# Performance work log

Measured on AMD Instinct MI355X. Metric: run time of the kernel, lower is better.

## Reference

```python
import jax, jax.numpy as jnp
import numpy as np

THETA_BASE = 10000.0

def rope(x, pos_offset=0):
    # x: (B, S, D), D even. Rotates interleaved (even, odd) dim pairs.
    B, S, D = x.shape
    pos = jnp.arange(pos_offset, pos_offset + S, dtype=jnp.float32)[:, None]  # (S,1)
    p = jnp.arange(D // 2, dtype=jnp.float32)  # p-1 in source, 0-indexed here
    theta = pos * (THETA_BASE ** (-2.0 * p / D))  # (S, D//2)
    sin_t, cos_t = jnp.sin(theta), jnp.cos(theta)
    x1, x2 = x[..., 0::2], x[..., 1::2]
    r1 = x1 * cos_t - x2 * sin_t
    r2 = x1 * sin_t + x2 * cos_t
    return jnp.stack((r1, r2), axis=-1).reshape(B, S, D)

def setup_inputs() -> dict:
    key = jax.random.key(0)
    k1, k2, k3, k4 = jax.random.split(key, 4)
    B, S, E, Dh = 4, 4096, 2048, 128
    return {
        "x": jax.random.normal(k1, (B, S, E), dtype=jnp.float32),
        "W_Q": jax.random.normal(k2, (E, Dh), dtype=jnp.float32) / np.sqrt(E),
        "W_K": jax.random.normal(k3, (E, Dh), dtype=jnp.float32) / np.sqrt(E),
        "W_V": jax.random.normal(k4, (E, Dh), dtype=jnp.float32) / np.sqrt(E),
    }

def reference(x, W_Q, W_K, W_V):
    d_h = W_Q.shape[1]
    past_len = 0  # kv_cache is None (prefill)
    Q = rope(x @ W_Q, pos_offset=past_len)  # NOTE: source ropes Q and V, not K
    K = x @ W_K
    V = rope(x @ W_V, pos_offset=past_len)
    scores = jnp.einsum('bqd,bkd->bqk', Q, K) / jnp.sqrt(jnp.float32(d_h))
    S_q, S_total = scores.shape[-2], scores.shape[-1]
    i = jnp.arange(S_q)[:, None] + past_len
    j = jnp.arange(S_total)[None, :]
    causal = j <= i  # (S_q, S_total) bool
    masked = jnp.where(causal[None, :, :], scores, jnp.float32(-jnp.inf))
    attn = jax.nn.softmax(masked, axis=-1)
    return jnp.einsum('bqk,bkd->bqd', attn, V)
```

## Files before the change

kernel.cpp:

```cpp
#include <hip/hip_runtime.h>
#include <hip/hip_bf16.h>
#include <stdint.h>

#define S_LEN 4096
#define E_DIM 2048
#define DH    128

typedef __bf16 bf16_t;
typedef bf16_t bf16x8 __attribute__((ext_vector_type(8)));
typedef float  f32x4  __attribute__((ext_vector_type(4)));

__device__ __forceinline__ unsigned short f2bf(float f) {
  union { float f; uint32_t u; } v; v.f = f;
  uint32_t u = v.u;
  uint32_t r = (u + 0x7fffu + ((u >> 16) & 1u)) >> 16;
  return (unsigned short)r;
}

__device__ __forceinline__ bf16x8 ld_bf16x8(const unsigned short* p) {
  return *(const bf16x8*)p;
}

__device__ __forceinline__ f32x4 mfma16(bf16x8 a, bf16x8 b, f32x4 c) {
  return __builtin_amdgcn_mfma_f32_16x16x32_bf16(a, b, c, 0, 0, 0);
}

__device__ __forceinline__ void gload16(const void* gsrc, void* ldst) {
  __builtin_amdgcn_global_load_lds(
      (const __attribute__((address_space(1))) uint32_t*)gsrc,
      (__attribute__((address_space(3))) uint32_t*)ldst, 16, 0, 0);
}

__global__ __launch_bounds__(256) void prep_kernel(
    const float* __restrict__ WQ, const float* __restrict__ WK,
    const float* __restrict__ WV,
    float2* __restrict__ trig, unsigned short* __restrict__ Wt)
{
  const int bx  = blockIdx.x;
  const int tid = threadIdx.x;
  if (bx < 1024) {
    const int idx = bx * 256 + tid;
    const int pos = idx >> 6, p = idx & 63;
    const float freq = powf(10000.0f, -(float)p / 64.0f);
    float sv, cv;
    sincosf((float)pos * freq, &sv, &cv);
    trig[idx] = make_float2(cv, sv);
    return;
  }
  __shared__ float lds[64][65];
  const int t   = bx - 1024;
  const int z   = t >> 6;
  const int rem = t & 63;
  const int k0  = (rem >> 1) * 64;
  const int n0  = (rem & 1) * 64;
  const float* W = (z == 0) ? WQ : ((z == 1) ? WK : WV);
  #pragma unroll
  for (int pass = 0; pass < 4; pass++) {
    const int r  = pass * 16 + (tid >> 4);
    const int c4 = (tid & 15) * 4;
    float4 v = *(const float4*)(W + (size_t)(k0 + r) * 128 + n0 + c4);
    lds[c4 + 0][r] = v.x; lds[c4 + 1][r] = v.y;
    lds[c4 + 2][r] = v.z; lds[c4 + 3][r] = v.w;
  }
  __syncthreads();
  #pragma unroll
  for (int pass = 0; pass < 4; pass++) {
    const int n  = pass * 16 + (tid >> 4);
    const int k4 = (tid & 15) * 4;
    ushort4 pk;
    pk.x = f2bf(lds[n][k4 + 0]); pk.y = f2bf(lds[n][k4 + 1]);
    pk.z = f2bf(lds[n][k4 + 2]); pk.w = f2bf(lds[n][k4 + 3]);
    *(ushort4*)(Wt + (size_t)(z * 128 + n0 + n) * E_DIM + k0 + k4) = pk;
  }
}

__global__ __launch_bounds__(256, 3) void proj_kernel(
    const float* __restrict__ x, const unsigned short* __restrict__ Wt,
    const float2* __restrict__ trig,
    unsigned short* __restrict__ Qb, unsigned short* __restrict__ Kb,
    unsigned short* __restrict__ Vt)
{
  __shared__ __align__(16) uint8_t Abuf[2 * 128 * 128];
  __shared__ __align__(16) uint8_t Bbuf[2 * 96 * 64];

  const int tid  = threadIdx.x;
  const int lane = tid & 63, w2 = tid >> 6;
  const int wr = w2 & 1, wc = w2 >> 1;
  const int col = lane & 15, kg = lane >> 4;

  const int m0 = blockIdx.x * 128;
  const int p  = blockIdx.y;

  f32x4 acc[4][3];
  #pragma unroll
  for (int i = 0; i < 4; i++)
    #pragma unroll
    for (int j = 0; j < 3; j++) acc[i][j] = (f32x4){0.f, 0.f, 0.f, 0.f};

  const int ar  = lane >> 3;
  const int acb = (lane & 7) * 16;
  const int br  = lane >> 2;
  const int bcb = (lane & 3) * 16;

  #define STAGE(K0, BUF)                                                      \
    do {                                                                      \
      uint8_t* Ad = Abuf + (BUF) * 16384 + w2 * 4096;                         \
      _Pragma("unroll")                                                       \
      for (int c = 0; c < 4; c++) {                                           \
        const int row = w2 * 32 + c * 8 + ar;                                 \
        const int src = acb ^ ((row & 7) << 4);                               \
        gload16((const char*)x + ((size_t)(m0 + row) * E_DIM + (K0)) * 4 + src,\
                Ad + c * 1024);                                               \
      }                                                                       \
      _Pragma("unroll")                                                       \
      for (int c = 0; c < 6; c++) {                                           \
        if ((c & 3) == w2) {                                                  \
          const int row = c * 16 + br;                                        \
          const int src = bcb ^ ((row & 3) << 4);                             \
          gload16((const char*)Wt +                                           \
                      ((size_t)(p * 96 + row) * E_DIM + (K0)) * 2 + src,      \
                  Bbuf + (BUF) * 6144 + c * 1024);                            \
        }                                                                     \
      }                                                                       \
    } while (0)

  STAGE(0, 0);
  __syncthreads();

  int cur = 0;
  for (int t = 0; t < 64; t++) {
    if (t < 63) STAGE((t + 1) * 32, cur ^ 1);

    const uint8_t* Ab = Abuf + cur * 16384;
    const uint8_t* Bb = Bbuf + cur * 6144;

    bf16x8 af[4];
    #pragma unroll
    for (int i = 0; i < 4; i++) {
      const int row = wr * 64 + i * 16 + col;
      const int sw  = (row & 7) << 4;
      float4 lo = *(const float4*)(Ab + row * 128 + ((kg * 32) ^ sw));
      float4 hi = *(const float4*)(Ab + row * 128 + ((kg * 32 + 16) ^ sw));
      bf16x8 a;
      a[0] = (bf16_t)lo.x; a[1] = (bf16_t)lo.y;
      a[2] = (bf16_t)lo.z; a[3] = (bf16_t)lo.w;
      a[4] = (bf16_t)hi.x; a[5] = (bf16_t)hi.y;
      a[6] = (bf16_t)hi.z; a[7] = (bf16_t)hi.w;
      af[i] = a;
    }
    __builtin_amdgcn_s_setprio(1);
    #pragma unroll
    for (int ns = 0; ns < 3; ns++) {
      const int n = wc * 48 + ns * 16 + col;
      bf16x8 bf = *(const bf16x8*)(Bb + n * 64 + ((kg * 16) ^ ((n & 3) << 4)));
      #pragma unroll
      for (int i = 0; i < 4; i++)
        acc[i][ns] = mfma16(af[i], bf, acc[i][ns]);
    }
    __builtin_amdgcn_s_setprio(0);
    __syncthreads();
    cur ^= 1;
  }
  #undef STAGE

  #pragma unroll
  for (int i = 0; i < 4; i++) {
    const int mbase = m0 + wr * 64 + i * 16 + kg * 4;
    const int spos  = mbase & 4095;
    const int bb    = mbase >> 12;
    #pragma unroll
    for (int ns = 0; ns < 3; ns++) {
      const int n = p * 96 + wc * 48 + ns * 16 + col;
      const int z = n >> 7, d = n & 127;
      f32x4 v = acc[i][ns];
      if (z == 1) {
        #pragma unroll
        for (int r = 0; r < 4; r++)
          Kb[(size_t)(mbase + r) * DH + d] = f2bf(v[r]);
      } else {
        const float sgn  = (d & 1) ? 1.0f : -1.0f;
        const int   pidx = d >> 1;
        float ov[4];
        #pragma unroll
        for (int r = 0; r < 4; r++) {
          float  pv = __shfl_xor(v[r], 1, 64);
          float2 cs = trig[(spos + r) * 64 + pidx];
          ov[r] = v[r] * cs.x + sgn * pv * cs.y;
        }
        if (z == 0) {
          #pragma unroll
          for (int r = 0; r < 4; r++)
            Qb[(size_t)(mbase + r) * DH + d] =
                f2bf(ov[r] * 0.08838834764831845f);
        } else {
          ushort4 pk;
          pk.x = f2bf(ov[0]); pk.y = f2bf(ov[1]);
          pk.z = f2bf(ov[2]); pk.w = f2bf(ov[3]);
          *(ushort4*)(Vt + ((size_t)(bb * DH + d)) * S_LEN + spos) = pk;
        }
      }
    }
  }
}

__global__ __launch_bounds__(256, 2) void flash_kernel(
    const unsigned short* __restrict__ Qb, const unsigned short* __restrict__ Kb,
    const unsigned short* __restrict__ Vt, float* __restrict__ out)
{
  __shared__ __align__(16) unsigned short Ktile[128 * 128];
  __shared__ __align__(16) unsigned short Vtile[128 * 128];
  __shared__ __align__(16) unsigned short Plds[4][16][72];

  const int bid  = blockIdx.x;
  const int half = bid >> 8, rb = bid & 255;
  const int qi   = half ? (127 - (rb >> 1)) : (rb >> 1);
  const int b    = (rb & 1) | (half << 1);
  const int q0   = qi * 32;

  const int tid = threadIdx.x;
  const int lane = tid & 63, w = tid >> 6;
  const int h   = w & 1;
  const int kvh = w >> 1;
  const int col = lane & 15, kg = lane >> 4;

  bf16x8 qf[4];
  {
    const unsigned short* qrow =
        Qb + (size_t)(b * S_LEN + q0 + h * 16 + col) * DH;
    #pragma unroll
    for (int kk = 0; kk < 4; kk++)
      qf[kk] = ld_bf16x8(qrow + kk * 32 + kg * 8);
  }

  f32x4 o[8];
  #pragma unroll
  for (int i = 0; i < 8; i++) o[i] = (f32x4){0.f, 0.f, 0.f, 0.f};
  float mrow[4] = {-1e30f, -1e30f, -1e30f, -1e30f};
  float lrow[4] = {0.f, 0.f, 0.f, 0.f};

  const char* Kbase = (const char*)(Kb + (size_t)b * S_LEN * DH);
  const char* Vbase = (const char*)(Vt + (size_t)b * DH * S_LEN);

  const int r_off = lane >> 4, colb = (lane & 15) * 16;

  for (int kv0 = 0; kv0 < q0 + 32; kv0 += 128) {
    #pragma unroll
    for (int c = 0; c < 8; c++) {
      const int row = w * 32 + c * 4 + r_off;
      const int src = colb ^ ((row & 7) << 4);
      gload16(Kbase + (size_t)(kv0 + row) * 256 + src,
              (char*)Ktile + w * 8192 + c * 1024);
    }
    #pragma unroll
    for (int c = 0; c < 8; c++) {
      const int d   = w * 32 + c * 4 + r_off;
      const int src = colb ^ ((d & 7) << 4);
      gload16(Vbase + (size_t)d * 8192 + (size_t)kv0 * 2 + src,
              (char*)Vtile + w * 8192 + c * 1024);
    }
    __syncthreads();

    f32x4 st[4];
    __builtin_amdgcn_s_setprio(1);
    #pragma unroll
    for (int kb = 0; kb < 4; kb++) {
      f32x4 sacc = (f32x4){0.f, 0.f, 0.f, 0.f};
      const int krow = kvh * 64 + kb * 16 + col;
      #pragma unroll
      for (int kk = 0; kk < 4; kk++) {
        bf16x8 kf = *(const bf16x8*)((const char*)Ktile + krow * 256 +
                                     ((kk * 64 + kg * 16) ^ ((krow & 7) << 4)));
        sacc = mfma16(qf[kk], kf, sacc);
      }
      st[kb] = sacc;
    }
    __builtin_amdgcn_s_setprio(0);

    if (kv0 + 127 > q0) {
      #pragma unroll
      for (int kb = 0; kb < 4; kb++) {
        const int key = kv0 + kvh * 64 + kb * 16 + col;
        #pragma unroll
        for (int r = 0; r < 4; r++) {
          const int q = q0 + h * 16 + kg * 4 + r;
          if (key > q) st[kb][r] = -1e30f;
        }
      }
    }

    float scale[4];
    #pragma unroll
    for (int r = 0; r < 4; r++) {
      float mx = fmaxf(fmaxf(st[0][r], st[1][r]), fmaxf(st[2][r], st[3][r]));
      #pragma unroll
      for (int off = 1; off < 16; off <<= 1)
        mx = fmaxf(mx, __shfl_xor(mx, off, 64));
      const float mnew = fmaxf(mrow[r], mx);
      scale[r] = __expf(mrow[r] - mnew);
      mrow[r] = mnew;
      float psum = 0.f;
      #pragma unroll
      for (int kb = 0; kb < 4; kb++) {
        float pexp = __expf(st[kb][r] - mnew);
        st[kb][r] = pexp;
        psum += pexp;
      }
      lrow[r] = lrow[r] * scale[r] + psum;
    }
    #pragma unroll
    for (int nt = 0; nt < 8; nt++)
      #pragma unroll
      for (int r = 0; r < 4; r++)
        o[nt][r] *= scale[r];

    #pragma unroll
    for (int kb = 0; kb < 4; kb++)
      #pragma unroll
      for (int r = 0; r < 4; r++)
        Plds[w][kg * 4 + r][kb * 16 + col] = f2bf(st[kb][r]);

    __builtin_amdgcn_s_setprio(1);
    #pragma unroll
    for (int kc = 0; kc < 2; kc++) {
      bf16x8 pa = ld_bf16x8(&Plds[w][col][kc * 32 + kg * 8]);
      #pragma unroll
      for (int nt = 0; nt < 8; nt++) {
        const int vrow = nt * 16 + col;
        bf16x8 vf = *(const bf16x8*)((const char*)Vtile + vrow * 256 +
            ((kvh * 128 + kc * 64 + kg * 16) ^ ((vrow & 7) << 4)));
        o[nt] = mfma16(pa, vf, o[nt]);
      }
    }
    __builtin_amdgcn_s_setprio(0);
    __syncthreads();
  }

  float lfull[4];
  #pragma unroll
  for (int r = 0; r < 4; r++) {
    float l = lrow[r];
    #pragma unroll
    for (int off = 1; off < 16; off <<= 1)
      l += __shfl_xor(l, off, 64);
    lfull[r] = l;
  }

  float* Olds = (float*)Ktile;
  float* Ml   = (float*)Vtile;
  #pragma unroll
  for (int nt = 0; nt < 8; nt++)
    #pragma unroll
    for (int r = 0; r < 4; r++)
      Olds[(w * 16 + kg * 4 + r) * 128 + nt * 16 + col] = o[nt][r];
  if (col == 0) {
    #pragma unroll
    for (int r = 0; r < 4; r++) {
      Ml[w * 16 + kg * 4 + r]      = mrow[r];
      Ml[64 + w * 16 + kg * 4 + r] = lfull[r];
    }
  }
  __syncthreads();
  if (w < 2) {
    #pragma unroll
    for (int r = 0; r < 4; r++) {
      const int row = kg * 4 + r;
      const float m1 = Ml[w * 16 + row],        l1 = Ml[64 + w * 16 + row];
      const float m2 = Ml[(w + 2) * 16 + row],  l2 = Ml[64 + (w + 2) * 16 + row];
      const float mf = fmaxf(m1, m2);
      const float w1 = __expf(m1 - mf), wgt2 = __expf(m2 - mf);
      const float inv = 1.0f / (l1 * w1 + l2 * wgt2);
      float* orow = out + (size_t)(b * S_LEN + q0 + w * 16 + row) * DH;
      #pragma unroll
      for (int nt = 0; nt < 8; nt++) {
        const float v1 = Olds[(w * 16 + row) * 128 + nt * 16 + col];
        const float v2 = Olds[((w + 2) * 16 + row) * 128 + nt * 16 + col];
        orow[nt * 16 + col] = (v1 * w1 + v2 * wgt2) * inv;
      }
    }
  }
}

extern "C" void kernel_launch(void* const* d_in, const int* in_sizes, int n_in,
                              void* d_out, int out_size, void* d_ws, size_t ws_size,
                              hipStream_t stream) {
  const float* x  = (const float*)d_in[0];
  const float* WQ = (const float*)d_in[1];
  const float* WK = (const float*)d_in[2];
  const float* WV = (const float*)d_in[3];
  float* out = (float*)d_out;

  char* ws = (char*)d_ws;
  float2*         trig = (float2*)(ws);
  unsigned short* Wt   = (unsigned short*)(ws + (2u << 20));
  unsigned short* Qb   = (unsigned short*)(ws + (4u << 20));
  unsigned short* Kb   = (unsigned short*)(ws + (8u << 20));
  unsigned short* Vt   = (unsigned short*)(ws + (12u << 20));

  hipLaunchKernelGGL(prep_kernel, dim3(1216), dim3(256), 0, stream,
                     WQ, WK, WV, trig, Wt);
  hipLaunchKernelGGL(proj_kernel, dim3(128, 4), dim3(256), 0, stream,
                     x, Wt, trig, Qb, Kb, Vt);
  hipLaunchKernelGGL(flash_kernel, dim3(512), dim3(256), 0, stream,
                     Qb, Kb, Vt, out);
}
```

Measured before the change: 142.4 us.

## Convert x tile to bf16 before LDS and double K-step per iteration

The projection GEMM now loads fp32 x tiles into registers and converts them to bf16 once while writing them into LDS, instead of storing fp32 in LDS and converting on every fragment read. The K tile doubles to 64 per iteration, halving the number of barriers, and the W tile layout widens to match. Launch bounds drop to 2 blocks per SM to make room for the extra register staging (8 float4 per thread). This trades fewer LDS bytes and conversions for higher register pressure and lower occupancy.

```diff
diff --git a/kernel.cpp b/kernel.cpp
--- a/kernel.cpp
+++ b/kernel.cpp
@@ -74,14 +74,14 @@
   }
 }
 
-__global__ __launch_bounds__(256, 3) void proj_kernel(
+__global__ __launch_bounds__(256, 2) void proj_kernel(
     const float* __restrict__ x, const unsigned short* __restrict__ Wt,
     const float2* __restrict__ trig,
     unsigned short* __restrict__ Qb, unsigned short* __restrict__ Kb,
     unsigned short* __restrict__ Vt)
 {
-  __shared__ __align__(16) uint8_t Abuf[2 * 128 * 128];
-  __shared__ __align__(16) uint8_t Bbuf[2 * 96 * 64];
+  __shared__ __align__(16) uint8_t Abuf[2][128 * 128];
+  __shared__ __align__(16) uint8_t Bbuf[2][96 * 128];
 
   const int tid  = threadIdx.x;
   const int lane = tid & 63, w2 = tid >> 6;
@@ -97,71 +97,88 @@
     #pragma unroll
     for (int j = 0; j < 3; j++) acc[i][j] = (f32x4){0.f, 0.f, 0.f, 0.f};
 
-  const int ar  = lane >> 3;
-  const int acb = (lane & 7) * 16;
-  const int br  = lane >> 2;
-  const int bcb = (lane & 3) * 16;
-
-  #define STAGE(K0, BUF)                                                      \
+  const int a_r = lane >> 4;
+  const int a_c = (lane & 15) * 4;
+  const int b_r  = lane >> 3;
+  const int b_cb = (lane & 7) * 16;
+
+  float4 a_reg[8];
+
+  #define ALOAD(K0)                                                           \
     do {                                                                      \
-      uint8_t* Ad = Abuf + (BUF) * 16384 + w2 * 4096;                         \
       _Pragma("unroll")                                                       \
-      for (int c = 0; c < 4; c++) {                                           \
-        const int row = w2 * 32 + c * 8 + ar;                                 \
-        const int src = acb ^ ((row & 7) << 4);                               \
-        gload16((const char*)x + ((size_t)(m0 + row) * E_DIM + (K0)) * 4 + src,\
-                Ad + c * 1024);                                               \
-      }                                                                       \
-      _Pragma("unroll")                                                       \
-      for (int c = 0; c < 6; c++) {                                           \
-        if ((c & 3) == w2) {                                                  \
-          const int row = c * 16 + br;                                        \
-          const int src = bcb ^ ((row & 3) << 4);                             \
-          gload16((const char*)Wt +                                           \
-                      ((size_t)(p * 96 + row) * E_DIM + (K0)) * 2 + src,      \
-                  Bbuf + (BUF) * 6144 + c * 1024);                            \
-        }                                                                     \
+      for (int j = 0; j < 8; j++) {                                           \
+        const int row = w2 * 32 + j * 4 + a_r;                                \
+        a_reg[j] = *(const float4*)(x + (size_t)(m0 + row) * E_DIM + (K0) + a_c);\
       }                                                                       \
     } while (0)
 
-  STAGE(0, 0);
+  #define BSTAGE(K0, BUF)                                                     \
+    do {                                                                      \
+      _Pragma("unroll")                                                       \
+      for (int c = 0; c < 3; c++) {                                           \
+        const int seg = w2 * 3 + c;                                           \
+        const int row = seg * 8 + b_r;                                        \
+        const int src = b_cb ^ ((row & 7) << 4);                              \
+        gload16((const char*)Wt + ((size_t)(p * 96 + row) * E_DIM + (K0)) * 2 + src,\
+                &Bbuf[BUF][seg * 1024]);                                      \
+      }                                                                       \
+    } while (0)
+
+  #define AWRITE(BUF)                                                         \
+    do {                                                                      \
+      _Pragma("unroll")                                                       \
+      for (int j = 0; j < 8; j++) {                                           \
+        const int row = w2 * 32 + j * 4 + a_r;                                \
+        ushort4 h;                                                            \
+        h.x = f2bf(a_reg[j].x); h.y = f2bf(a_reg[j].y);                       \
+        h.z = f2bf(a_reg[j].z); h.w = f2bf(a_reg[j].w);                       \
+        const int dst = (a_c * 2) ^ ((row & 7) << 4);                         \
+        *(ushort4*)(&Abuf[BUF][row * 128 + dst]) = h;                         \
+      }                                                                       \
+    } while (0)
+
+  ALOAD(0);
+  BSTAGE(0, 0);
+  AWRITE(0);
   __syncthreads();
 
   int cur = 0;
-  for (int t = 0; t < 64; t++) {
-    if (t < 63) STAGE((t + 1) * 32, cur ^ 1);
-
-    const uint8_t* Ab = Abuf + cur * 16384;
-    const uint8_t* Bb = Bbuf + cur * 6144;
-
-    bf16x8 af[4];
-    #pragma unroll
-    for (int i = 0; i < 4; i++) {
-      const int row = wr * 64 + i * 16 + col;
-      const int sw  = (row & 7) << 4;
-      float4 lo = *(const float4*)(Ab + row * 128 + ((kg * 32) ^ sw));
-      float4 hi = *(const float4*)(Ab + row * 128 + ((kg * 32 + 16) ^ sw));
-      bf16x8 a;
-      a[0] = (bf16_t)lo.x; a[1] = (bf16_t)lo.y;
-      a[2] = (bf16_t)lo.z; a[3] = (bf16_t)lo.w;
-      a[4] = (bf16_t)hi.x; a[5] = (bf16_t)hi.y;
-      a[6] = (bf16_t)hi.z; a[7] = (bf16_t)hi.w;
-      af[i] = a;
-    }
+  for (int t = 0; t < 32; t++) {
+    if (t < 31) {
+      ALOAD((t + 1) * 64);
+      BSTAGE((t + 1) * 64, cur ^ 1);
+    }
+
     __builtin_amdgcn_s_setprio(1);
     #pragma unroll
-    for (int ns = 0; ns < 3; ns++) {
-      const int n = wc * 48 + ns * 16 + col;
-      bf16x8 bf = *(const bf16x8*)(Bb + n * 64 + ((kg * 16) ^ ((n & 3) << 4)));
-      #pragma unroll
-      for (int i = 0; i < 4; i++)
-        acc[i][ns] = mfma16(af[i], bf, acc[i][ns]);
+    for (int kk = 0; kk < 2; kk++) {
+      bf16x8 af[4];
+      #pragma unroll
+      for (int i = 0; i < 4; i++) {
+        const int row = wr * 64 + i * 16 + col;
+        af[i] = *(const bf16x8*)(&Abuf[cur][row * 128 +
+                 ((kk * 64 + kg * 16) ^ ((row & 7) << 4))]);
+      }
+      #pragma unroll
+      for (int ns = 0; ns < 3; ns++) {
+        const int n = wc * 48 + ns * 16 + col;
+        bf16x8 bf = *(const bf16x8*)(&Bbuf[cur][n * 128 +
+                    ((kk * 64 + kg * 16) ^ ((n & 7) << 4))]);
+        #pragma unroll
+        for (int i = 0; i < 4; i++)
+          acc[i][ns] = mfma16(af[i], bf, acc[i][ns]);
+      }
     }
     __builtin_amdgcn_s_setprio(0);
+
+    if (t < 31) AWRITE(cur ^ 1);
     __syncthreads();
     cur ^= 1;
   }
-  #undef STAGE
+  #undef ALOAD
+  #undef BSTAGE
+  #undef AWRITE
 
   #pragma unroll
   for (int i = 0; i < 4; i++) {
```

Result: faster. 136.1 us (-4.5%).
